# Kernel optimization log

Hardware: AMD Instinct MI355X
Metric: run time of the kernel (lower is better)

## Reference

```python
import jax, jax.numpy as jnp
import numpy as np

V, E, H, B, S, L = 32000, 512, 1024, 128, 256, 2


def setup_inputs() -> dict:
    key = jax.random.key(0)
    ks = jax.random.split(key, 20)
    sc = 0.02
    n = lambda k, shape: jax.random.normal(k, shape, dtype=jnp.float32) * sc
    return {
        "input_ids": jax.random.randint(ks[0], (B,), 0, V),
        "h0": jax.random.normal(ks[1], (L, B, H), dtype=jnp.float32),
        "c0": jax.random.normal(ks[2], (L, B, H), dtype=jnp.float32),
        "enc_out": jax.random.normal(ks[3], (S, B, H), dtype=jnp.float32),
        "emb": n(ks[4], (V, E)),
        "w_ih0": n(ks[5], (4 * H, E)),
        "w_hh0": n(ks[6], (4 * H, H)),
        "b_ih0": n(ks[7], (4 * H,)),
        "b_hh0": n(ks[8], (4 * H,)),
        "w_ih1": n(ks[9], (4 * H, H)),
        "w_hh1": n(ks[10], (4 * H, H)),
        "b_ih1": n(ks[11], (4 * H,)),
        "b_hh1": n(ks[12], (4 * H,)),
        "attn_w": n(ks[13], (H, H)),
        "attn_b": n(ks[14], (H,)),
        "concat_w": n(ks[15], (H, 2 * H)),
        "concat_b": n(ks[16], (H,)),
        "out_w": n(ks[17], (V, H)),
        "out_b": n(ks[18], (V,)),
    }


def _lstm_step(x, h, c, w_ih, w_hh, b_ih, b_hh):
    # PyTorch gate order: i, f, g, o
    g = x @ w_ih.T + b_ih + h @ w_hh.T + b_hh  # [B, 4H]
    i, f, gg, o = jnp.split(g, 4, axis=-1)
    c_new = jax.nn.sigmoid(f) * c + jax.nn.sigmoid(i) * jnp.tanh(gg)
    h_new = jax.nn.sigmoid(o) * jnp.tanh(c_new)
    return h_new, c_new


def reference(input_ids, h0, c0, enc_out, emb, w_ih0, w_hh0, b_ih0, b_hh0,
              w_ih1, w_hh1, b_ih1, b_hh1, attn_w, attn_b, concat_w, concat_b,
              out_w, out_b):
    x = emb[input_ids]  # [B, E] (dropout is identity in eval)
    h_0, c_0 = _lstm_step(x, h0[0], c0[0], w_ih0, w_hh0, b_ih0, b_hh0)
    h_1, c_1 = _lstm_step(h_0, h0[1], c0[1], w_ih1, w_hh1, b_ih1, b_hh1)
    rnn_out = h_1  # [B, H] == rnn_output.squeeze(0)
    # Luong general attention: scores[b,s] = <W enc[s,b], rnn_out[b]>
    e_proj = enc_out @ attn_w.T + attn_b          # [S, B, H]
    scores = jnp.einsum('sbh,bh->bs', e_proj, rnn_out)  # [B, S]
    attn = jax.nn.softmax(scores, axis=-1)
    context = jnp.einsum('bs,sbh->bh', attn, enc_out)   # [B, H]
    concat_out = jnp.tanh(
        jnp.concatenate([rnn_out, context], axis=-1) @ concat_w.T + concat_b)
    logits = concat_out @ out_w.T + out_b         # [B, V]
    h_new = jnp.stack([h_0, h_1])
    c_new = jnp.stack([c_0, c_1])
    return logits, h_new, c_new
```

## Files before the change

kernel.cpp:

```cpp
#include <hip/hip_runtime.h>
#include <hip/hip_bf16.h>
#include <cstddef>
#include <cstdint>

constexpr int Bv = 128;
constexpr int Sv = 256;
constexpr int Hv = 1024;
constexpr int Ev = 512;
constexpr int Vv = 32000;

typedef __attribute__((ext_vector_type(4))) float f32x4;
typedef __attribute__((ext_vector_type(8))) short short8;

__device__ __forceinline__ uint2 cvt4(float4 v) {
  union { __hip_bfloat162 b; unsigned u; } lo, hi;
  lo.b = __float22bfloat162_rn(float2{v.x, v.y});
  hi.b = __float22bfloat162_rn(float2{v.z, v.w});
  uint2 r;
  r.x = lo.u;
  r.y = hi.u;
  return r;
}
__device__ __forceinline__ unsigned short cvt1(float x) {
  union { __hip_bfloat16 b; unsigned short u; } c;
  c.b = __float2bfloat16(x);
  return c.u;
}

template <int BM, int BN, int SPLIT, int WTR, int GATHER, int MINW>
__global__ __launch_bounds__(256, MINW) void gemm_mfma(
    const int* __restrict__ ids,
    const float* __restrict__ A1, int lda1, int K1,
    const float* __restrict__ A2, int lda2, int K2,
    const float* __restrict__ W1, int ldw1,
    const float* __restrict__ W2, int ldw2,
    const float* __restrict__ bias1, const float* __restrict__ bias2,
    float* __restrict__ C, int ldc, int N) {
  constexpr int BK = 32, LP = 40;
  constexpr int WAVES_N = (BN >= 64) ? 2 : 1;
  constexpr int WAVES_M = 4 / WAVES_N;
  constexpr int WM = BM / WAVES_M;
  constexpr int FM = WM / 16;
  constexpr int FN = 2;
  constexpr int ACH = (BM * BK) / (4 * 256);
  constexpr int WCH = (BN * BK) / (4 * 256);

  __shared__ unsigned short Al[BM * LP];
  __shared__ unsigned short Wl[BN * LP];

  const int tid = threadIdx.x;
  const int wid = tid >> 6, lane = tid & 63;
  const int nBlock = blockIdx.x * BN;
  const int mBlock = blockIdx.y * BM;
  const int z = blockIdx.z;
  int wm, wn;
  if (WAVES_N == 2) { wm = (wid >> 1) * WM; wn = (wid & 1) * 32; }
  else              { wm = wid * WM;        wn = 0; }

  float4 av[ACH], wv[WCH];

  auto load_tile = [&](int kg) {
    const bool seg1 = kg < K1;
    const float* Wseg = seg1 ? W1 : W2;
    const int ldw = seg1 ? ldw1 : ldw2;
    const int kloc = seg1 ? kg : kg - K1;
#pragma unroll
    for (int i = 0; i < ACH; i++) {
      int c = tid + i * 256;
      int m = c >> 3, kq = (c & 7) << 2;
      const float* arow;
      if (seg1) {
        if (GATHER) arow = A1 + (size_t)ids[mBlock + m] * lda1;
        else        arow = A1 + (size_t)(mBlock + m) * lda1;
      } else {
        arow = A2 + (size_t)(mBlock + m) * lda2;
      }
      av[i] = *(const float4*)(arow + kloc + kq);
    }
    if (WTR) {
      int row = tid >> 3, colq = tid & 7;
      wv[0] = *(const float4*)(Wseg + (size_t)(kloc + row) * ldw + nBlock + colq * 4);
    } else {
#pragma unroll
      for (int i = 0; i < WCH; i++) {
        int c = tid + i * 256;
        int n = c >> 3, kq = (c & 7) << 2;
        wv[i] = *(const float4*)(Wseg + (size_t)(nBlock + n) * ldw + kloc + kq);
      }
    }
  };

  const int KT = K1 + K2;
  const int KS = KT / SPLIT;
  const int kbeg = z * KS;
  const int NS = KS / BK;
  load_tile(kbeg);
  f32x4 acc[FM][FN] = {};

  for (int step = 0; step < NS; ++step) {
    __syncthreads();
#pragma unroll
    for (int i = 0; i < ACH; i++) {
      int c = tid + i * 256;
      int m = c >> 3, kq = (c & 7) << 2;
      *(uint2*)&Al[m * LP + kq] = cvt4(av[i]);
    }
    if (WTR) {
      int row = tid >> 3, colq = tid & 7;
      Wl[(colq * 4 + 0) * LP + row] = cvt1(wv[0].x);
      Wl[(colq * 4 + 1) * LP + row] = cvt1(wv[0].y);
      Wl[(colq * 4 + 2) * LP + row] = cvt1(wv[0].z);
      Wl[(colq * 4 + 3) * LP + row] = cvt1(wv[0].w);
    } else {
#pragma unroll
      for (int i = 0; i < WCH; i++) {
        int c = tid + i * 256;
        int n = c >> 3, kq = (c & 7) << 2;
        *(uint2*)&Wl[n * LP + kq] = cvt4(wv[i]);
      }
    }
    __syncthreads();

    if (step + 1 < NS) load_tile(kbeg + (step + 1) * BK);

    const int klane = (lane >> 4) << 3;
    const int r = lane & 15;
    short8 af[FM], wf[FN];
#pragma unroll
    for (int f = 0; f < FM; f++)
      af[f] = *(const short8*)&Al[(wm + f * 16 + r) * LP + klane];
#pragma unroll
    for (int f = 0; f < FN; f++)
      wf[f] = *(const short8*)&Wl[(wn + f * 16 + r) * LP + klane];
#pragma unroll
    for (int fm = 0; fm < FM; fm++)
#pragma unroll
      for (int fn = 0; fn < FN; fn++)
        acc[fm][fn] = __builtin_amdgcn_mfma_f32_16x16x32_bf16(
            af[fm], wf[fn], acc[fm][fn], 0, 0, 0);
  }

  float* Cp = C + (size_t)z * gridDim.y * BM * ldc;
  const int col = lane & 15, rb = (lane >> 4) << 2;
#pragma unroll
  for (int fn = 0; fn < FN; fn++) {
    int n = nBlock + wn + fn * 16 + col;
    float bsum = 0.f;
    if (z == 0) {
      if (bias1) bsum += bias1[n];
      if (bias2) bsum += bias2[n];
    }
#pragma unroll
    for (int fm = 0; fm < FM; fm++) {
#pragma unroll
      for (int j = 0; j < 4; j++) {
        int m = mBlock + wm + fm * 16 + rb + j;
        Cp[(size_t)m * ldc + n] = acc[fm][fn][j] + bsum;
      }
    }
  }
}

template <int P>
__global__ void lstm_pw(const float* __restrict__ Gp,
                        const float* __restrict__ c_prev,
                        float* __restrict__ h_out,
                        float* __restrict__ c_out) {
  int i4 = blockIdx.x * 256 + threadIdx.x;
  int b = i4 >> 8, j4 = i4 & 255;
  float4 gi{}, gf{}, gg{}, go{};
#pragma unroll
  for (int p = 0; p < P; p++) {
    const float4* g = (const float4*)(Gp + (size_t)p * Bv * 4 * Hv + (size_t)b * 4096);
    float4 a = g[j4], bb = g[256 + j4], c = g[512 + j4], d = g[768 + j4];
    gi.x += a.x; gi.y += a.y; gi.z += a.z; gi.w += a.w;
    gf.x += bb.x; gf.y += bb.y; gf.z += bb.z; gf.w += bb.w;
    gg.x += c.x; gg.y += c.y; gg.z += c.z; gg.w += c.w;
    go.x += d.x; go.y += d.y; go.z += d.z; go.w += d.w;
  }
  float4 c4 = ((const float4*)c_prev)[i4];
  float4 h4, cn4;
  float* gip = &gi.x; float* gfp = &gf.x; float* ggp = &gg.x; float* gop = &go.x;
  float* cp = &c4.x; float* hp = &h4.x; float* cnp = &cn4.x;
#pragma unroll
  for (int u = 0; u < 4; u++) {
    float si = 1.f / (1.f + expf(-gip[u]));
    float sf = 1.f / (1.f + expf(-gfp[u]));
    float so = 1.f / (1.f + expf(-gop[u]));
    float cn = sf * cp[u] + si * tanhf(ggp[u]);
    hp[u] = so * tanhf(cn);
    cnp[u] = cn;
  }
  ((float4*)h_out)[i4] = h4;
  ((float4*)c_out)[i4] = cn4;
}

__global__ void scores_k(const float* __restrict__ enc,
                         const float* __restrict__ qp,
                         float* __restrict__ sc) {
  int blk = blockIdx.x;
  int b = blk >> 6, s4 = blk & 63;
  int t = threadIdx.x;
  __shared__ float qs[1024];
  {
    const float4* q0 = (const float4*)(qp + (size_t)b * Hv);
    const float4* q1 = (const float4*)(qp + 1 * Bv * Hv + (size_t)b * Hv);
    const float4* q2 = (const float4*)(qp + 2 * Bv * Hv + (size_t)b * Hv);
    const float4* q3 = (const float4*)(qp + 3 * Bv * Hv + (size_t)b * Hv);
    float4 a = q0[t], bq = q1[t], c = q2[t], d = q3[t];
    float4 s;
    s.x = a.x + bq.x + c.x + d.x; s.y = a.y + bq.y + c.y + d.y;
    s.z = a.z + bq.z + c.z + d.z; s.w = a.w + bq.w + c.w + d.w;
    ((float4*)qs)[t] = s;
  }
  __syncthreads();
  int wid = t >> 6, lane = t & 63;
  int s = s4 * 4 + wid;
  const float4* e4 = (const float4*)(enc + ((size_t)s * Bv + b) * Hv);
  const float4* q4 = (const float4*)qs;
  float sum = 0.f;
#pragma unroll
  for (int i = 0; i < 4; i++) {
    int idx = lane + i * 64;
    float4 e = e4[idx], qq = q4[idx];
    sum += e.x * qq.x + e.y * qq.y + e.z * qq.z + e.w * qq.w;
  }
#pragma unroll
  for (int o = 32; o; o >>= 1) sum += __shfl_xor(sum, o);
  if (lane == 0) sc[(size_t)b * Sv + s] = sum;
}

__global__ void context_k(const float* __restrict__ sc_in,
                          const float* __restrict__ enc,
                          float* __restrict__ ctx) {
  int blk = blockIdx.x;
  int b = blk >> 2, hc = (blk & 3) * 256;
  int t = threadIdx.x, lane = t & 63;
  __shared__ float a[256];
  __shared__ float redm[4], reds[4];
  float v = sc_in[(size_t)b * Sv + t];
  float m = v;
#pragma unroll
  for (int o = 32; o; o >>= 1) m = fmaxf(m, __shfl_xor(m, o));
  if (lane == 0) redm[t >> 6] = m;
  __syncthreads();
  m = fmaxf(fmaxf(redm[0], redm[1]), fmaxf(redm[2], redm[3]));
  float e = expf(v - m);
  float ssum = e;
#pragma unroll
  for (int o = 32; o; o >>= 1) ssum += __shfl_xor(ssum, o);
  if (lane == 0) reds[t >> 6] = ssum;
  __syncthreads();
  ssum = (reds[0] + reds[1]) + (reds[2] + reds[3]);
  a[t] = e / ssum;
  __syncthreads();

  float acc = 0.f;
  const float* ebase = enc + (size_t)b * Hv + hc + t;
#pragma unroll 8
  for (int s = 0; s < Sv; s++)
    acc += a[s] * ebase[(size_t)s * Bv * Hv];
  ctx[(size_t)b * Hv + hc + t] = acc;
}

__global__ void finish_cat(const float* __restrict__ catp,
                           float* __restrict__ cat) {
  int i4 = blockIdx.x * 256 + threadIdx.x;
  constexpr int ST = Bv * Hv / 4;
  const float4* p = (const float4*)catp;
  float4 a = p[i4], b = p[ST + i4], c = p[2 * ST + i4], d = p[3 * ST + i4];
  float4 r;
  r.x = tanhf(a.x + b.x + c.x + d.x);
  r.y = tanhf(a.y + b.y + c.y + d.y);
  r.z = tanhf(a.z + b.z + c.z + d.z);
  r.w = tanhf(a.w + b.w + c.w + d.w);
  ((float4*)cat)[i4] = r;
}

extern "C" void kernel_launch(void* const* d_in, const int* in_sizes, int n_in,
                              void* d_out, int out_size, void* d_ws,
                              size_t ws_size, hipStream_t stream) {
  const int*   ids      = (const int*)d_in[0];
  const float* h0       = (const float*)d_in[1];
  const float* c0       = (const float*)d_in[2];
  const float* enc      = (const float*)d_in[3];
  const float* emb      = (const float*)d_in[4];
  const float* w_ih0    = (const float*)d_in[5];
  const float* w_hh0    = (const float*)d_in[6];
  const float* b_ih0    = (const float*)d_in[7];
  const float* b_hh0    = (const float*)d_in[8];
  const float* w_ih1    = (const float*)d_in[9];
  const float* w_hh1    = (const float*)d_in[10];
  const float* b_ih1    = (const float*)d_in[11];
  const float* b_hh1    = (const float*)d_in[12];
  const float* attn_w   = (const float*)d_in[13];
  const float* attn_b   = (const float*)d_in[14];
  const float* concat_w = (const float*)d_in[15];
  const float* concat_b = (const float*)d_in[16];
  const float* out_w    = (const float*)d_in[17];
  const float* out_b    = (const float*)d_in[18];
  (void)attn_b;

  float* logits = (float*)d_out;
  float* hout   = logits + (size_t)Bv * Vv;
  float* cout   = hout + 2 * Bv * Hv;

  float* ws   = (float*)d_ws;
  float* G0p  = ws;
  float* G1p  = G0p + 3 * 524288;
  float* qp   = G1p + 4 * (size_t)524288;
  float* catp = qp + 4 * 131072;
  float* cat  = catp + 4 * 131072;
  float* ctx  = cat + 131072;
  float* sc   = ctx + 131072;

  const float* h_b = hout + Bv * Hv;

  gemm_mfma<64, 32, 3, 0, 1, 4><<<dim3(128, 2, 3), 256, 0, stream>>>(
      ids, emb, Ev, Ev, h0, Hv, Hv, w_ih0, Ev, w_hh0, Hv, b_ih0, b_hh0,
      G0p, 4 * Hv, 4 * Hv);
  lstm_pw<3><<<128, 256, 0, stream>>>(G0p, c0, hout, cout);
  gemm_mfma<64, 32, 4, 0, 0, 4><<<dim3(128, 2, 4), 256, 0, stream>>>(
      nullptr, hout, Hv, Hv, h0 + Bv * Hv, Hv, Hv, w_ih1, Hv, w_hh1, Hv,
      b_ih1, b_hh1, G1p, 4 * Hv, 4 * Hv);
  lstm_pw<4><<<128, 256, 0, stream>>>(G1p, c0 + Bv * Hv, hout + Bv * Hv,
                                      cout + Bv * Hv);
  gemm_mfma<64, 32, 4, 1, 0, 4><<<dim3(32, 2, 4), 256, 0, stream>>>(
      nullptr, h_b, Hv, Hv, nullptr, 0, 0, attn_w, Hv,
      nullptr, 0, nullptr, nullptr, qp, Hv, Hv);
  scores_k<<<8192, 256, 0, stream>>>(enc, qp, sc);
  context_k<<<512, 256, 0, stream>>>(sc, enc, ctx);
  gemm_mfma<64, 32, 4, 0, 0, 4><<<dim3(32, 2, 4), 256, 0, stream>>>(
      nullptr, h_b, Hv, Hv, ctx, Hv, Hv, concat_w, 2 * Hv,
      concat_w + Hv, 2 * Hv, concat_b, nullptr, catp, Hv, Hv);
  finish_cat<<<128, 256, 0, stream>>>(catp, cat);
  gemm_mfma<64, 64, 1, 0, 0, 4><<<dim3(500, 2, 1), 256, 0, stream>>>(
      nullptr, cat, Hv, Hv, nullptr, 0, 0, out_w, Hv, nullptr, 0,
      out_b, nullptr, logits, Vv, Vv);
}
```

Measured before the change: 179.8 us.

## Store concat output as bf16 and retile output projection to full-batch M tiles

The tanh of the concat layer is now written in bf16, and the final vocab projection GEMM loads its A operand straight as bf16 without converting. The output GEMM is retiled from 64x64 tiles over two M blocks to 128x32 tiles covering the whole batch, so each out_w tile is read once instead of twice. This is meant to cut redundant streaming of the large out_w matrix and the A-side conversion work. In exchange the N tile is narrower, there are more blocks, and each thread holds more A fragments.

```diff
diff --git a/kernel.cpp b/kernel.cpp
--- a/kernel.cpp
+++ b/kernel.cpp
@@ -27,7 +27,7 @@
   return c.u;
 }
 
-template <int BM, int BN, int SPLIT, int WTR, int GATHER, int MINW>
+template <int BM, int BN, int SPLIT, int WTR, int GATHER, int ABF16, int MINW>
 __global__ __launch_bounds__(256, MINW) void gemm_mfma(
     const int* __restrict__ ids,
     const float* __restrict__ A1, int lda1, int K1,
@@ -57,25 +57,37 @@
   if (WAVES_N == 2) { wm = (wid >> 1) * WM; wn = (wid & 1) * 32; }
   else              { wm = wid * WM;        wn = 0; }
 
-  float4 av[ACH], wv[WCH];
+  float4 av[ABF16 ? 1 : ACH];
+  uint4  av2[ABF16 ? (ACH / 2) : 1];
+  float4 wv[WCH];
 
   auto load_tile = [&](int kg) {
     const bool seg1 = kg < K1;
     const float* Wseg = seg1 ? W1 : W2;
     const int ldw = seg1 ? ldw1 : ldw2;
     const int kloc = seg1 ? kg : kg - K1;
-#pragma unroll
-    for (int i = 0; i < ACH; i++) {
-      int c = tid + i * 256;
-      int m = c >> 3, kq = (c & 7) << 2;
-      const float* arow;
-      if (seg1) {
-        if (GATHER) arow = A1 + (size_t)ids[mBlock + m] * lda1;
-        else        arow = A1 + (size_t)(mBlock + m) * lda1;
-      } else {
-        arow = A2 + (size_t)(mBlock + m) * lda2;
-      }
-      av[i] = *(const float4*)(arow + kloc + kq);
+    if (ABF16) {
+      const unsigned short* Ab = (const unsigned short*)A1;
+#pragma unroll
+      for (int i = 0; i < ACH / 2; i++) {
+        int c = tid + i * 256;
+        int m = c >> 2, ko = (c & 3) << 3;
+        av2[i] = *(const uint4*)(Ab + (size_t)(mBlock + m) * lda1 + kloc + ko);
+      }
+    } else {
+#pragma unroll
+      for (int i = 0; i < ACH; i++) {
+        int c = tid + i * 256;
+        int m = c >> 3, kq = (c & 7) << 2;
+        const float* arow;
+        if (seg1) {
+          if (GATHER) arow = A1 + (size_t)ids[mBlock + m] * lda1;
+          else        arow = A1 + (size_t)(mBlock + m) * lda1;
+        } else {
+          arow = A2 + (size_t)(mBlock + m) * lda2;
+        }
+        av[i] = *(const float4*)(arow + kloc + kq);
+      }
     }
     if (WTR) {
       int row = tid >> 3, colq = tid & 7;
@@ -99,11 +111,20 @@
 
   for (int step = 0; step < NS; ++step) {
     __syncthreads();
-#pragma unroll
-    for (int i = 0; i < ACH; i++) {
-      int c = tid + i * 256;
-      int m = c >> 3, kq = (c & 7) << 2;
-      *(uint2*)&Al[m * LP + kq] = cvt4(av[i]);
+    if (ABF16) {
+#pragma unroll
+      for (int i = 0; i < ACH / 2; i++) {
+        int c = tid + i * 256;
+        int m = c >> 2, ko = (c & 3) << 3;
+        *(uint4*)&Al[m * LP + ko] = av2[i];
+      }
+    } else {
+#pragma unroll
+      for (int i = 0; i < ACH; i++) {
+        int c = tid + i * 256;
+        int m = c >> 3, kq = (c & 7) << 2;
+        *(uint2*)&Al[m * LP + kq] = cvt4(av[i]);
+      }
     }
     if (WTR) {
       int row = tid >> 3, colq = tid & 7;
@@ -264,7 +285,7 @@
 }
 
 __global__ void finish_cat(const float* __restrict__ catp,
-                           float* __restrict__ cat) {
+                           unsigned short* __restrict__ catb) {
   int i4 = blockIdx.x * 256 + threadIdx.x;
   constexpr int ST = Bv * Hv / 4;
   const float4* p = (const float4*)catp;
@@ -274,7 +295,7 @@
   r.y = tanhf(a.y + b.y + c.y + d.y);
   r.z = tanhf(a.z + b.z + c.z + d.z);
   r.w = tanhf(a.w + b.w + c.w + d.w);
-  ((float4*)cat)[i4] = r;
+  *(uint2*)&catb[i4 * 4] = cvt4(r);
 }
 
 extern "C" void kernel_launch(void* const* d_in, const int* in_sizes, int n_in,
@@ -310,31 +331,31 @@
   float* G1p  = G0p + 3 * 524288;
   float* qp   = G1p + 4 * (size_t)524288;
   float* catp = qp + 4 * 131072;
-  float* cat  = catp + 4 * 131072;
-  float* ctx  = cat + 131072;
+  float* ctx  = catp + 4 * 131072;
   float* sc   = ctx + 131072;
+  unsigned short* catb = (unsigned short*)(sc + 32768);
 
   const float* h_b = hout + Bv * Hv;
 
-  gemm_mfma<64, 32, 3, 0, 1, 4><<<dim3(128, 2, 3), 256, 0, stream>>>(
+  gemm_mfma<64, 32, 3, 0, 1, 0, 4><<<dim3(128, 2, 3), 256, 0, stream>>>(
       ids, emb, Ev, Ev, h0, Hv, Hv, w_ih0, Ev, w_hh0, Hv, b_ih0, b_hh0,
       G0p, 4 * Hv, 4 * Hv);
   lstm_pw<3><<<128, 256, 0, stream>>>(G0p, c0, hout, cout);
-  gemm_mfma<64, 32, 4, 0, 0, 4><<<dim3(128, 2, 4), 256, 0, stream>>>(
+  gemm_mfma<64, 32, 4, 0, 0, 0, 4><<<dim3(128, 2, 4), 256, 0, stream>>>(
       nullptr, hout, Hv, Hv, h0 + Bv * Hv, Hv, Hv, w_ih1, Hv, w_hh1, Hv,
       b_ih1, b_hh1, G1p, 4 * Hv, 4 * Hv);
   lstm_pw<4><<<128, 256, 0, stream>>>(G1p, c0 + Bv * Hv, hout + Bv * Hv,
                                       cout + Bv * Hv);
-  gemm_mfma<64, 32, 4, 1, 0, 4><<<dim3(32, 2, 4), 256, 0, stream>>>(
+  gemm_mfma<64, 32, 4, 1, 0, 0, 4><<<dim3(32, 2, 4), 256, 0, stream>>>(
       nullptr, h_b, Hv, Hv, nullptr, 0, 0, attn_w, Hv,
       nullptr, 0, nullptr, nullptr, qp, Hv, Hv);
   scores_k<<<8192, 256, 0, stream>>>(enc, qp, sc);
   context_k<<<512, 256, 0, stream>>>(sc, enc, ctx);
-  gemm_mfma<64, 32, 4, 0, 0, 4><<<dim3(32, 2, 4), 256, 0, stream>>>(
+  gemm_mfma<64, 32, 4, 0, 0, 0, 4><<<dim3(32, 2, 4), 256, 0, stream>>>(
       nullptr, h_b, Hv, Hv, ctx, Hv, Hv, concat_w, 2 * Hv,
       concat_w + Hv, 2 * Hv, concat_b, nullptr, catp, Hv, Hv);
-  finish_cat<<<128, 256, 0, stream>>>(catp, cat);
-  gemm_mfma<64, 64, 1, 0, 0, 4><<<dim3(500, 2, 1), 256, 0, stream>>>(
-      nullptr, cat, Hv, Hv, nullptr, 0, 0, out_w, Hv, nullptr, 0,
-      out_b, nullptr, logits, Vv, Vv);
-}
+  finish_cat<<<128, 256, 0, stream>>>(catp, catb);
+  gemm_mfma<128, 32, 1, 0, 0, 1, 4><<<dim3(1000, 1, 1), 256, 0, stream>>>(
+      nullptr, (const float*)catb, Hv, Hv, nullptr, 0, 0, out_w, Hv,
+      nullptr, 0, out_b, nullptr, logits, Vv, Vv);
+}
```

Measured after the change: 226.7 us. +26.1%, slower.
